# Performance work log

Hardware: AMD Instinct MI355X
Metric: run time of the kernel (lower is better)

The kernel has to match this reference:

```python
import jax, jax.numpy as jnp
import numpy as np

NH = 4        # n_head
L_TOPK = 16   # AWG top-k l
DEC = 2       # dec_layers
EPS = 1e-6


def _ln(x, g, b):
    m = jnp.mean(x, -1, keepdims=True)
    v = jnp.mean((x - m) ** 2, -1, keepdims=True)
    return (x - m) * jax.lax.rsqrt(v + EPS) * g + b


def _heads(x, W):
    B, L, C = x.shape
    return (x @ W).reshape(B, L, NH, C // NH).transpose(0, 2, 1, 3)  # [B,H,L,dk]


def _softmax_attn(qh, kh):
    dk = qh.shape[-1]
    logits = jnp.einsum('bhqd,bhkd->bhqk', qh / jnp.sqrt(jnp.float32(dk)), kh)
    return jax.nn.softmax(logits, axis=-1)


def cross_attn_block(q, k, v, Wq, Wk, Wv, Wo, g, b):
    B, Lq, C = q.shape
    a = _softmax_attn(_heads(q, Wq), _heads(k, Wk))
    o = jnp.einsum('bhqk,bhkd->bhqd', a, _heads(v, Wv))
    o = o.transpose(0, 2, 1, 3).reshape(B, Lq, C) @ Wo
    return _ln(o + q, g, b)


def awg_attn_block(q, k, v, Wq, Wk, Wv, Wo, g, b):
    # top-k attention-weight-gating: keep weights >= l-th largest, renormalize
    B, Lq, C = q.shape
    a = _softmax_attn(_heads(q, Wq), _heads(k, Wk))
    thr = jax.lax.top_k(a, L_TOPK)[0][..., -1:]          # [B,H,Lq,1]
    w = a * (a >= thr).astype(a.dtype)
    w = w / jnp.sum(w, -1, keepdims=True)
    o = jnp.einsum('bhqk,bhkd->bhqd', w, _heads(v, Wv))
    o = o.transpose(0, 2, 1, 3).reshape(B, Lq, C) @ Wo
    return _ln(o + q, g, b)


def setup_inputs() -> dict:
    key = jax.random.key(0)
    ks = jax.random.split(key, 32)
    B, Lq, Lk, C, F = 4, 3000, 750, 64, 256
    s = 1.0 / np.sqrt(C)
    sf = 1.0 / np.sqrt(F)
    d = {}
    d['q'] = jax.random.normal(ks[0], (B, Lq, C), jnp.float32)
    d['enc'] = jax.random.normal(ks[1], (B, Lk, C), jnp.float32)
    # cross_attn_layer params
    for i, n in enumerate(['cal_Wq', 'cal_Wk', 'cal_Wv', 'cal_Wo']):
        d[n] = jax.random.normal(ks[2 + i], (C, C), jnp.float32) * s
    d['cal_ln1_g'] = jnp.ones((C,), jnp.float32)
    d['cal_ln1_b'] = jnp.zeros((C,), jnp.float32)
    d['cal_W1'] = jax.random.normal(ks[6], (C, F), jnp.float32) * s
    d['cal_b1'] = jnp.zeros((F,), jnp.float32)
    d['cal_W2'] = jax.random.normal(ks[7], (F, C), jnp.float32) * sf
    d['cal_b2'] = jnp.zeros((C,), jnp.float32)
    d['cal_ln2_g'] = jnp.ones((C,), jnp.float32)
    d['cal_ln2_b'] = jnp.zeros((C,), jnp.float32)
    # stacked MGAN params [DEC, ...]
    d['m_ln_g'] = jnp.ones((DEC, C), jnp.float32)
    d['m_ln_b'] = jnp.zeros((DEC, C), jnp.float32)
    d['m_fc1_W'] = jax.random.normal(ks[8], (DEC, C, C), jnp.float32) * s
    d['m_fc1_b'] = jnp.zeros((DEC, C), jnp.float32)
    d['m_fc2_W'] = jax.random.normal(ks[9], (DEC, C, C), jnp.float32) * s
    d['m_fc2_b'] = jnp.zeros((DEC, C), jnp.float32)
    for i, n in enumerate(['m_Wq', 'm_Wk', 'm_Wv', 'm_Wo']):
        d[n] = jax.random.normal(ks[10 + i], (DEC, C, C), jnp.float32) * s
    d['m_aln_g'] = jnp.ones((DEC, C), jnp.float32)
    d['m_aln_b'] = jnp.zeros((DEC, C), jnp.float32)
    d['fc_W'] = jax.random.normal(ks[14], (C, 1), jnp.float32) * s
    d['fc_b'] = jnp.zeros((1,), jnp.float32)
    return d


def reference(q, enc, cal_Wq, cal_Wk, cal_Wv, cal_Wo, cal_ln1_g, cal_ln1_b,
              cal_W1, cal_b1, cal_W2, cal_b2, cal_ln2_g, cal_ln2_b,
              m_ln_g, m_ln_b, m_fc1_W, m_fc1_b, m_fc2_W, m_fc2_b,
              m_Wq, m_Wk, m_Wv, m_Wo, m_aln_g, m_aln_b, fc_W, fc_b):
    # cross_attn_layer: attention + FFN + LN (dropout = identity in eval)
    x = cross_attn_block(q, enc, enc, cal_Wq, cal_Wk, cal_Wv, cal_Wo, cal_ln1_g, cal_ln1_b)
    ffn = jax.nn.relu(x @ cal_W1 + cal_b1) @ cal_W2 + cal_b2
    x = _ln(ffn + x, cal_ln2_g, cal_ln2_b)
    # MGAN decoder layers (rep_KV: k,v = encoder output)
    for i in range(DEC):
        qn = _ln(x, m_ln_g[i], m_ln_b[i])
        sg = jax.nn.sigmoid(qn @ m_fc1_W[i] + m_fc1_b[i]) * (qn @ m_fc2_W[i] + m_fc2_b[i])
        awg = awg_attn_block(sg, enc, enc, m_Wq[i], m_Wk[i], m_Wv[i], m_Wo[i],
                             m_aln_g[i], m_aln_b[i])
        # GLU(cat(sg, awg)) = sg * sigmoid(awg)
        x = qn + sg * jax.nn.sigmoid(awg)
    # label_type='p' head
    return jax.nn.sigmoid(x @ fc_W + fc_b)  # [B, Lq, 1]
```

## Files before the change

### kernel.cpp

```cpp
#include <hip/hip_runtime.h>
#include <hip/hip_bf16.h>

using bf16 = __hip_bfloat16;

#define DEV_INLINE __device__ __forceinline__

constexpr int B_  = 4;
constexpr int LQ  = 3000;
constexpr int LK  = 750;
constexpr int NH_ = 4;
constexpr float EPSF = 1e-6f;

constexpr int PITCH = 753;

constexpr size_t WS_KV = 0;
constexpr size_t WS_XB = 1152000;
constexpr size_t WS_QP = 1920000;
constexpr size_t WS_AO = 2688000;
constexpr size_t WS_QN = 3456000;
constexpr size_t WS_SG = 4224000;

typedef _Float16 half2_t __attribute__((ext_vector_type(2)));
typedef _Float16 half4_t __attribute__((ext_vector_type(4)));
typedef float    f32x4   __attribute__((ext_vector_type(4)));

#define MFMA16(a, b, c) __builtin_amdgcn_mfma_f32_16x16x16f16((a), (b), (c), 0, 0, 0)

DEV_INLINE float sigmoidf(float x) { return 1.f / (1.f + __expf(-x)); }

DEV_INLINE unsigned int packh2(float a, float b) {
  half2_t h = { (_Float16)a, (_Float16)b };
  unsigned int u; __builtin_memcpy(&u, &h, 4); return u;
}
DEV_INLINE half2_t u2h(unsigned int u) {
  half2_t h; __builtin_memcpy(&h, &u, 4); return h;
}
DEV_INLINE unsigned short f2h(float f) {
  _Float16 h = (_Float16)f;
  unsigned short u; __builtin_memcpy(&u, &h, 2); return u;
}
DEV_INLINE half4_t h4_from(const unsigned short* p) {
  unsigned int lo = *(const unsigned int*)p;
  unsigned int hi = *(const unsigned int*)(p + 2);
  unsigned long long v = ((unsigned long long)hi << 32) | lo;
  half4_t h; __builtin_memcpy(&h, &v, 8); return h;
}
DEV_INLINE float dot2(unsigned int kw, half2_t qh, float acc) {
  return __builtin_amdgcn_fdot2(u2h(kw), qh, acc, false);
}

DEV_INLINE unsigned int f2sort(float f) {
  int ib = __float_as_int(f);
  return (unsigned int)(ib ^ ((ib >> 31) | 0x80000000));
}
DEV_INLINE float sort2f(unsigned int u) {
  const int ib = (u & 0x80000000u) ? (int)(u ^ 0x80000000u) : (int)~u;
  return __int_as_float(ib);
}

DEV_INLINE unsigned int bcastu(unsigned int v) {
  return (unsigned int)__builtin_amdgcn_readfirstlane((int)v);
}

DEV_INLINE void sort64u_desc4(unsigned int v[4]) {
  const int lane = threadIdx.x & 63;
  #pragma unroll
  for (int k = 2; k <= 64; k <<= 1) {
    #pragma unroll
    for (int j = k >> 1; j > 0; j >>= 1) {
      const bool takeMax = ((lane & j) == 0) == ((lane & k) == 0);
      #pragma unroll
      for (int r = 0; r < 4; ++r) {
        const unsigned int o = __shfl_xor(v[r], j);
        v[r] = (takeMax == (v[r] > o)) ? v[r] : o;
      }
    }
  }
}
DEV_INLINE void sort64p_desc4(unsigned long long v[4]) {
  const int lane = threadIdx.x & 63;
  #pragma unroll
  for (int k = 2; k <= 64; k <<= 1) {
    #pragma unroll
    for (int j = k >> 1; j > 0; j >>= 1) {
      const bool takeMax = ((lane & j) == 0) == ((lane & k) == 0);
      #pragma unroll
      for (int r = 0; r < 4; ++r) {
        const unsigned long long o = __shfl_xor(v[r], j);
        v[r] = (takeMax == (v[r] > o)) ? v[r] : o;
      }
    }
  }
}

DEV_INLINE float row_ln(float v, float g, float b) {
  float s1 = v, s2 = v * v;
  #pragma unroll
  for (int off = 32; off > 0; off >>= 1) {
    s1 += __shfl_xor(s1, off);
    s2 += __shfl_xor(s2, off);
  }
  const float m   = s1 * (1.f / 64.f);
  const float var = s2 * (1.f / 64.f) - m * m;
  return (v - m) * rsqrtf(var + EPSF) * g + b;
}

__global__ __launch_bounds__(256) void kvq_proj_kernel(
    const float* __restrict__ enc, const float* __restrict__ q,
    const float* __restrict__ calWq,
    const float* __restrict__ calWk, const float* __restrict__ calWv,
    const float* __restrict__ mWk, const float* __restrict__ mWv,
    float* __restrict__ kv, float* __restrict__ qp)
{
  const int y = blockIdx.y;
  if (y < 6 && blockIdx.x >= 188) return;
  __shared__ float Wl[64 * 65];
  __shared__ float xs[16][64];
  const int t = threadIdx.x, rr = t >> 6, cc = t & 63;
  const float* W;
  const float* src;
  float* dst;
  float scale = 1.f;
  int nrows = 3000;
  switch (y) {
    case 0: W = calWk; src = enc; dst = kv;               break;
    case 1: W = calWv; src = enc; dst = kv + 192000;      break;
    case 2: W = mWk;        src = enc; dst = kv + 384000; break;
    case 3: W = mWv;        src = enc; dst = kv + 576000; break;
    case 4: W = mWk + 4096; src = enc; dst = kv + 768000; break;
    case 5: W = mWv + 4096; src = enc; dst = kv + 960000; break;
    default: W = calWq; src = q; dst = qp; scale = 0.25f; nrows = 12000; break;
  }
  const bool packK = (y == 2) || (y == 4);
  for (int i = t; i < 4096; i += 256) Wl[(i >> 6) * 65 + (i & 63)] = W[i];
  const int base = blockIdx.x * 16;
  for (int i = t; i < 1024; i += 256) {
    const int grow = base + (i >> 6);
    xs[i >> 6][i & 63] = (grow < nrows) ? src[(size_t)grow * 64 + (i & 63)] : 0.f;
  }
  __syncthreads();
  #pragma unroll
  for (int p = 0; p < 4; ++p) {
    const int row = p * 4 + rr;
    const int grow = base + row;
    float acc = 0.f;
    #pragma unroll
    for (int c = 0; c < 64; ++c) acc = fmaf(xs[row][c], Wl[c * 65 + cc], acc);
    if (packK) {
      const float accN = __shfl_xor(acc, 1);
      if (!(cc & 1) && grow < nrows)
        ((unsigned int*)dst)[(size_t)grow * 32 + (cc >> 1)] = packh2(acc, accN);
    } else if (grow < nrows) {
      dst[(size_t)grow * 64 + cc] = acc * scale;
    }
  }
}

__global__ __launch_bounds__(256) void cross_attn_kernel(
    const float* __restrict__ qp, const float* __restrict__ kp,
    const float* __restrict__ vp, float* __restrict__ ao)
{
  extern __shared__ char smem[];
  unsigned short* Kl = (unsigned short*)smem;
  unsigned short* Vt = Kl + 750 * 18;
  unsigned short* Pt = Vt + 16 * 754;

  const int t = threadIdx.x;
  const int h = blockIdx.y, b = blockIdx.z;
  const float* kslab = kp + (size_t)(b * LK) * 64 + h * 16;
  const float* vslab = vp + (size_t)(b * LK) * 64 + h * 16;

  for (int k = t; k < LK; k += 256) {
    const float4* ks = (const float4*)(kslab + (size_t)k * 64);
    const float4* vs = (const float4*)(vslab + (size_t)k * 64);
    unsigned int* kr = (unsigned int*)(Kl + k * 18);
    #pragma unroll
    for (int q4 = 0; q4 < 4; ++q4) {
      float4 a = ks[q4], v = vs[q4];
      kr[q4 * 2]     = packh2(a.x, a.y);
      kr[q4 * 2 + 1] = packh2(a.z, a.w);
      Vt[(q4 * 4 + 0) * 754 + k] = f2h(v.x);
      Vt[(q4 * 4 + 1) * 754 + k] = f2h(v.y);
      Vt[(q4 * 4 + 2) * 754 + k] = f2h(v.z);
      Vt[(q4 * 4 + 3) * 754 + k] = f2h(v.w);
    }
  }
  if (t < 32) Vt[(t & 15) * 754 + 750 + (t >> 4)] = 0;
  __syncthreads();

  const int wave = t >> 6, lane = t & 63;
  const int col = lane & 15, quad = lane >> 4;
  const int qbase = blockIdx.x * 64 + wave * 16;
  unsigned short* Pt_w = Pt + wave * 288;

  int qrow = qbase + col; if (qrow >= LQ) qrow = LQ - 1;
  const float* qptr = qp + ((size_t)(b * LQ + qrow)) * 64 + h * 16 + quad * 4;
  half4_t aQ;
  {
    unsigned long long v = ((unsigned long long)packh2(qptr[2], qptr[3]) << 32)
                         | packh2(qptr[0], qptr[1]);
    __builtin_memcpy(&aQ, &v, 8);
  }

  f32x4 O = {0.f, 0.f, 0.f, 0.f};
  float Zp[4] = {0.f, 0.f, 0.f, 0.f};
  const f32x4 zeroC = {0.f, 0.f, 0.f, 0.f};

  for (int tile = 0; tile < 47; ++tile) {
    const int key = tile * 16 + col;
    const half4_t bK = h4_from(Kl + key * 18 + quad * 4);
    f32x4 S = MFMA16(aQ, bK, zeroC);
    const bool valid = key < LK;
    float e0 = valid ? __expf(S[0]) : 0.f;
    float e1 = valid ? __expf(S[1]) : 0.f;
    float e2 = valid ? __expf(S[2]) : 0.f;
    float e3 = valid ? __expf(S[3]) : 0.f;
    Zp[0] += e0; Zp[1] += e1; Zp[2] += e2; Zp[3] += e3;
    Pt_w[(quad * 4 + 0) * 18 + col] = f2h(e0);
    Pt_w[(quad * 4 + 1) * 18 + col] = f2h(e1);
    Pt_w[(quad * 4 + 2) * 18 + col] = f2h(e2);
    Pt_w[(quad * 4 + 3) * 18 + col] = f2h(e3);
    const half4_t aP = h4_from(Pt_w + col * 18 + quad * 4);
    const half4_t bV = h4_from(Vt + col * 754 + tile * 16 + quad * 4);
    O = MFMA16(aP, bV, O);
  }

  #pragma unroll
  for (int r = 0; r < 4; ++r) {
    float z = Zp[r];
    z += __shfl_xor(z, 1);
    z += __shfl_xor(z, 2);
    z += __shfl_xor(z, 4);
    z += __shfl_xor(z, 8);
    Zp[r] = z;
  }

  #pragma unroll
  for (int r = 0; r < 4; ++r) {
    const int orow = qbase + quad * 4 + r;
    if (orow < LQ)
      ao[((size_t)(b * LQ + orow)) * 64 + h * 16 + col] = O[r] / Zp[r];
  }
}

__global__ __launch_bounds__(512) void awg_attn_kernel(
    const float* __restrict__ qp, const unsigned int* __restrict__ kp,
    const float* __restrict__ vp, float* __restrict__ ao)
{
  extern __shared__ char smem[];
  uint2*              KT2  = (uint2*)smem;
  unsigned long long* cand = (unsigned long long*)(smem + 4 * PITCH * 8);
  float*              selW = (float*)(smem + 4 * PITCH * 8 + 16384);
  unsigned short*     selK = (unsigned short*)(smem + 4 * PITCH * 8 + 16384 + 3072);

  const int t = threadIdx.x;
  const int h = blockIdx.y, b = blockIdx.z;
  const unsigned int* kslab = kp + ((size_t)(b * LK)) * 32 + h * 8;

  for (int k = t; k < LK; k += 512) {
    const uint2* ks = (const uint2*)(kslab + (size_t)k * 32);
    #pragma unroll
    for (int d4 = 0; d4 < 4; ++d4) KT2[d4 * PITCH + k] = ks[d4];
  }
  __syncthreads();

  const int wave = t >> 6, lane = t & 63;
  const unsigned long long below = (1ull << lane) - 1ull;
  unsigned long long* cd = cand + wave * 256;
  float*              sW = selW + wave * 96;
  unsigned short*     sK = selK + wave * 96;

  sW[lane] = -3.0e38f; sK[lane] = 0;
  if (lane < 32) { sW[64 + lane] = -3.0e38f; sK[64 + lane] = 0; }
  #pragma unroll
  for (int r = 0; r < 4; ++r) cd[r * 64 + lane] = 0ull;

  const int r0 = blockIdx.x * 32 + wave * 4;
  int r0r = r0; if (r0r > LQ - 4) r0r = LQ - 4;
  const float* qrow = qp + ((size_t)(b * LQ + r0r)) * 64 + h * 16;
  unsigned int qw[4][8];
  #pragma unroll
  for (int r = 0; r < 4; ++r) {
    #pragma unroll
    for (int i = 0; i < 8; ++i)
      qw[r][i] = bcastu(packh2(qrow[r * 64 + 2 * i], qrow[r * 64 + 2 * i + 1]));
  }

  float lg[4][12];
  #pragma unroll
  for (int tt = 0; tt < 12; ++tt) {
    const int k = lane + (tt << 6);
    if (tt < 11 || k < LK) {
      float a0 = 0.f, a1 = 0.f, a2 = 0.f, a3 = 0.f;
      #pragma unroll
      for (int d4 = 0; d4 < 4; ++d4) {
        const uint2 w = KT2[d4 * PITCH + k];
        a0 = dot2(w.x, u2h(qw[0][2 * d4]), a0); a0 = dot2(w.y, u2h(qw[0][2 * d4 + 1]), a0);
        a1 = dot2(w.x, u2h(qw[1][2 * d4]), a1); a1 = dot2(w.y, u2h(qw[1][2 * d4 + 1]), a1);
        a2 = dot2(w.x, u2h(qw[2][2 * d4]), a2); a2 = dot2(w.y, u2h(qw[2][2 * d4 + 1]), a2);
        a3 = dot2(w.x, u2h(qw[3][2 * d4]), a3); a3 = dot2(w.y, u2h(qw[3][2 * d4 + 1]), a3);
      }
      lg[0][tt] = a0; lg[1][tt] = a1; lg[2][tt] = a2; lg[3][tt] = a3;
    } else {
      lg[0][tt] = -3.0e38f; lg[1][tt] = -3.0e38f;
      lg[2][tt] = -3.0e38f; lg[3][tt] = -3.0e38f;
    }
  }

  unsigned int hs[4];
  #pragma unroll
  for (int r = 0; r < 4; ++r) {
    float m = lg[r][0];
    #pragma unroll
    for (int tt = 1; tt < 12; ++tt) m = fmaxf(m, lg[r][tt]);
    hs[r] = f2sort(m);
  }

  sort64u_desc4(hs);
  unsigned int L[4];
  #pragma unroll
  for (int r = 0; r < 4; ++r) L[r] = __shfl(hs[r], 15);

  int cb[4] = {0, 0, 0, 0};
  #pragma unroll
  for (int tt = 0; tt < 12; ++tt) {
    const int k = lane + (tt << 6);
    #pragma unroll
    for (int r = 0; r < 4; ++r) {
      const unsigned int s = f2sort(lg[r][tt]);
      const bool p = s >= L[r];
      const unsigned long long m = __ballot(p);
      if (p) {
        const int pos = cb[r] + (int)__popcll(m & below);
        if (pos < 64)
          cd[r * 64 + pos] = ((unsigned long long)s << 16) | (unsigned int)k;
      }
      cb[r] += (int)__popcll(m);
    }
  }

  unsigned long long sv[4];
  #pragma unroll
  for (int r = 0; r < 4; ++r) sv[r] = cd[r * 64 + lane];
  sort64p_desc4(sv);

  unsigned int su[4], cu15[4];
  float Mv[4];
  #pragma unroll
  for (int r = 0; r < 4; ++r) {
    su[r]   = (unsigned int)(sv[r] >> 16);
    cu15[r] = __shfl(su[r], 15);
    Mv[r]   = sort2f(__shfl(su[r], 0));
  }
  #pragma unroll
  for (int r = 0; r < 4; ++r) {
    if (lane < 24 && su[r] >= cu15[r]) {
      sW[r * 24 + lane] = sort2f(su[r]);
      sK[r * 24 + lane] = (unsigned short)(sv[r] & 0xFFFFull);
    }
  }

  const int dd = lane & 15;
  const int rsel = lane >> 4;
  const float ref = (rsel == 0) ? Mv[0] : (rsel == 1) ? Mv[1] : (rsel == 2) ? Mv[2] : Mv[3];
  const float* cwr = sW + rsel * 24;
  const unsigned short* cir = sK + rsel * 24;
  const float* vbase = vp + (size_t)(b * LK) * 64 + h * 16 + dd;
  float acc = 0.f, Z = 0.f;
  #pragma unroll
  for (int j = 0; j < 24; ++j) {
    const float e = __expf(cwr[j] - ref);
    Z += e;
    acc = fmaf(e, vbase[(size_t)cir[j] * 64], acc);
  }
  if (r0 + rsel < LQ)
    ao[((size_t)(b * LQ + r0 + rsel)) * 64 + h * 16 + dd] = acc / Z;
}

__global__ __launch_bounds__(256) void cross_ffn_kernel(
    const float* __restrict__ ao, const float* __restrict__ qres,
    const float* __restrict__ Wo,
    const float* __restrict__ g1, const float* __restrict__ b1n,
    const float* __restrict__ W1, const float* __restrict__ bb1,
    const float* __restrict__ W2, const float* __restrict__ bb2,
    const float* __restrict__ g2, const float* __restrict__ b2n,
    float* __restrict__ xout)
{
  __shared__ float xs[8][64];
  __shared__ float hs[8][256];
  const int t = threadIdx.x, rr = t >> 6, cc = t & 63;
  const size_t base = (size_t)blockIdx.x * 8;
  for (int i = t; i < 512; i += 256) xs[i >> 6][i & 63] = ao[base * 64 + i];
  __syncthreads();
  float acc[2];
  #pragma unroll
  for (int p = 0; p < 2; ++p) {
    const int row = p * 4 + rr;
    float a = 0.f;
    #pragma unroll
    for (int c = 0; c < 64; ++c) a = fmaf(xs[row][c], Wo[c * 64 + cc], a);
    acc[p] = a + qres[(base + row) * 64 + cc];
  }
  __syncthreads();
  #pragma unroll
  for (int p = 0; p < 2; ++p) {
    const int row = p * 4 + rr;
    xs[row][cc] = row_ln(acc[p], g1[cc], b1n[cc]);
  }
  __syncthreads();
  {
    float hv[8];
    #pragma unroll
    for (int r = 0; r < 8; ++r) hv[r] = 0.f;
    #pragma unroll 8
    for (int c = 0; c < 64; ++c) {
      const float w = W1[c * 256 + t];
      #pragma unroll
      for (int r = 0; r < 8; ++r) hv[r] = fmaf(xs[r][c], w, hv[r]);
    }
    const float bb = bb1[t];
    #pragma unroll
    for (int r = 0; r < 8; ++r) hs[r][t] = fmaxf(hv[r] + bb, 0.f);
  }
  __syncthreads();
  float acc2[2];
  #pragma unroll
  for (int p = 0; p < 2; ++p) acc2[p] = bb2[cc];
  #pragma unroll 8
  for (int c = 0; c < 256; ++c) {
    const float w = W2[c * 64 + cc];
    acc2[0] = fmaf(hs[rr][c], w, acc2[0]);
    acc2[1] = fmaf(hs[4 + rr][c], w, acc2[1]);
  }
  #pragma unroll
  for (int p = 0; p < 2; ++p) {
    const int row = p * 4 + rr;
    const float a = acc2[p] + xs[row][cc];
    xout[(base + row) * 64 + cc] = row_ln(a, g2[cc], b2n[cc]);
  }
}

__global__ __launch_bounds__(256) void mgan_pre_kernel(
    const float* __restrict__ x, const float* __restrict__ lng,
    const float* __restrict__ lnb, const float* __restrict__ W1,
    const float* __restrict__ bb1, const float* __restrict__ W2,
    const float* __restrict__ bb2, const float* __restrict__ Wq,
    float* __restrict__ qn, float* __restrict__ sg, float* __restrict__ qp)
{
  __shared__ float qs[8][64];
  __shared__ float sgs[8][64];
  const int t = threadIdx.x, rr = t >> 6, cc = t & 63;
  const size_t base = (size_t)blockIdx.x * 8;
  #pragma unroll
  for (int p = 0; p < 2; ++p) {
    const int row = p * 4 + rr;
    const float v = x[(base + row) * 64 + cc];
    const float qv = row_ln(v, lng[cc], lnb[cc]);
    qn[(base + row) * 64 + cc] = qv;
    qs[row][cc] = qv;
  }
  __syncthreads();
  float d1[2], d2[2];
  #pragma unroll
  for (int p = 0; p < 2; ++p) { d1[p] = bb1[cc]; d2[p] = bb2[cc]; }
  #pragma unroll 4
  for (int c = 0; c < 64; ++c) {
    const float w1 = W1[c * 64 + cc];
    const float w2 = W2[c * 64 + cc];
    #pragma unroll
    for (int p = 0; p < 2; ++p) {
      const float xv = qs[p * 4 + rr][c];
      d1[p] = fmaf(xv, w1, d1[p]);
      d2[p] = fmaf(xv, w2, d2[p]);
    }
  }
  #pragma unroll
  for (int p = 0; p < 2; ++p) {
    const int row = p * 4 + rr;
    const float sv = sigmoidf(d1[p]) * d2[p];
    sg[(base + row) * 64 + cc] = sv;
    sgs[row][cc] = sv;
  }
  __syncthreads();
  #pragma unroll
  for (int p = 0; p < 2; ++p) {
    const int row = p * 4 + rr;
    float a = 0.f;
    #pragma unroll
    for (int c = 0; c < 64; ++c) a = fmaf(sgs[row][c], Wq[c * 64 + cc], a);
    qp[(base + row) * 64 + cc] = a * 0.25f;
  }
}

__global__ __launch_bounds__(256) void out_pre_kernel(
    const float* __restrict__ ao, const float* __restrict__ sg,
    const float* __restrict__ qn, const float* __restrict__ Wo,
    const float* __restrict__ g_, const float* __restrict__ b_,
    const float* __restrict__ lng, const float* __restrict__ lnb,
    const float* __restrict__ W1, const float* __restrict__ bb1,
    const float* __restrict__ W2, const float* __restrict__ bb2,
    const float* __restrict__ Wq,
    float* __restrict__ qn_out, float* __restrict__ sg_out,
    float* __restrict__ qp_out)
{
  __shared__ float xs[8][64];
  __shared__ float sgs[8][64];
  const int t = threadIdx.x, rr = t >> 6, cc = t & 63;
  const size_t base = (size_t)blockIdx.x * 8;
  for (int i = t; i < 512; i += 256) xs[i >> 6][i & 63] = ao[base * 64 + i];
  __syncthreads();
  float accp[2], sgv[2];
  #pragma unroll
  for (int p = 0; p < 2; ++p) {
    const int row = p * 4 + rr;
    const size_t idx = (base + row) * 64 + cc;
    float a = 0.f;
    #pragma unroll
    for (int c = 0; c < 64; ++c) a = fmaf(xs[row][c], Wo[c * 64 + cc], a);
    sgv[p] = sg[idx];
    accp[p] = a + sgv[p];
  }
  __syncthreads();
  #pragma unroll
  for (int p = 0; p < 2; ++p) {
    const int row = p * 4 + rr;
    const size_t idx = (base + row) * 64 + cc;
    const float awg = row_ln(accp[p], g_[cc], b_[cc]);
    const float xv = qn[idx] + sgv[p] * sigmoidf(awg);
    const float qv = row_ln(xv, lng[cc], lnb[cc]);
    qn_out[idx] = qv;
    xs[row][cc] = qv;
  }
  __syncthreads();
  float d1[2], d2[2];
  #pragma unroll
  for (int p = 0; p < 2; ++p) { d1[p] = bb1[cc]; d2[p] = bb2[cc]; }
  #pragma unroll 4
  for (int c = 0; c < 64; ++c) {
    const float w1 = W1[c * 64 + cc];
    const float w2 = W2[c * 64 + cc];
    #pragma unroll
    for (int p = 0; p < 2; ++p) {
      const float xv = xs[p * 4 + rr][c];
      d1[p] = fmaf(xv, w1, d1[p]);
      d2[p] = fmaf(xv, w2, d2[p]);
    }
  }
  __syncthreads();
  #pragma unroll
  for (int p = 0; p < 2; ++p) {
    const int row = p * 4 + rr;
    const size_t idx = (base + row) * 64 + cc;
    const float sv = sigmoidf(d1[p]) * d2[p];
    sg_out[idx] = sv;
    sgs[row][cc] = sv;
  }
  __syncthreads();
  #pragma unroll
  for (int p = 0; p < 2; ++p) {
    const int row = p * 4 + rr;
    float a = 0.f;
    #pragma unroll
    for (int c = 0; c < 64; ++c) a = fmaf(sgs[row][c], Wq[c * 64 + cc], a);
    qp_out[(base + row) * 64 + cc] = a * 0.25f;
  }
}

__global__ __launch_bounds__(256) void out_final_kernel(
    const float* __restrict__ ao, const float* __restrict__ sg,
    const float* __restrict__ qn, const float* __restrict__ Wo,
    const float* __restrict__ g_, const float* __restrict__ b_,
    const float* __restrict__ fw, const float* __restrict__ fb,
    float* __restrict__ out)
{
  __shared__ float xs[8][64];
  const int t = threadIdx.x, rr = t >> 6, cc = t & 63;
  const size_t base = (size_t)blockIdx.x * 8;
  for (int i = t; i < 512; i += 256) xs[i >> 6][i & 63] = ao[base * 64 + i];
  __syncthreads();
  #pragma unroll
  for (int p = 0; p < 2; ++p) {
    const int row = p * 4 + rr;
    const size_t idx = (base + row) * 64 + cc;
    float a = 0.f;
    #pragma unroll
    for (int c = 0; c < 64; ++c) a = fmaf(xs[row][c], Wo[c * 64 + cc], a);
    const float sgv = sg[idx];
    a += sgv;
    const float awg = row_ln(a, g_[cc], b_[cc]);
    const float xv = qn[idx] + sgv * sigmoidf(awg);
    float v = xv * fw[cc];
    #pragma unroll
    for (int off = 32; off > 0; off >>= 1) v += __shfl_xor(v, off);
    if (cc == 0) out[base + row] = sigmoidf(v + fb[0]);
  }
}

extern "C" void kernel_launch(void* const* d_in, const int* in_sizes, int n_in,
                              void* d_out, int out_size, void* d_ws, size_t ws_size,
                              hipStream_t stream) {
  (void)in_sizes; (void)n_in; (void)out_size; (void)ws_size;

  const float* q     = (const float*)d_in[0];
  const float* enc   = (const float*)d_in[1];
  const float* calWq = (const float*)d_in[2];
  const float* calWk = (const float*)d_in[3];
  const float* calWv = (const float*)d_in[4];
  const float* calWo = (const float*)d_in[5];
  const float* ln1g  = (const float*)d_in[6];
  const float* ln1b  = (const float*)d_in[7];
  const float* W1    = (const float*)d_in[8];
  const float* b1v   = (const float*)d_in[9];
  const float* W2    = (const float*)d_in[10];
  const float* b2v   = (const float*)d_in[11];
  const float* ln2g  = (const float*)d_in[12];
  const float* ln2b  = (const float*)d_in[13];
  const float* mlng  = (const float*)d_in[14];
  const float* mlnb  = (const float*)d_in[15];
  const float* mfc1W = (const float*)d_in[16];
  const float* mfc1b = (const float*)d_in[17];
  const float* mfc2W = (const float*)d_in[18];
  const float* mfc2b = (const float*)d_in[19];
  const float* mWq   = (const float*)d_in[20];
  const float* mWk   = (const float*)d_in[21];
  const float* mWv   = (const float*)d_in[22];
  const float* mWo   = (const float*)d_in[23];
  const float* malng = (const float*)d_in[24];
  const float* malnb = (const float*)d_in[25];
  const float* fcW   = (const float*)d_in[26];
  const float* fcb   = (const float*)d_in[27];
  float* out = (float*)d_out;

  float* ws  = (float*)d_ws;
  float* kv  = ws + WS_KV;
  float* qp  = ws + WS_QP;
  float* aob = ws + WS_AO;
  float* qnb = ws + WS_QN;
  float* sgb = ws + WS_SG;
  float* xb  = ws + WS_XB;

  const size_t crossLds = (750 * 18 + 16 * 754 + 4 * 288) * 2;
  const size_t awgLds   = 4 * PITCH * 8 + 16384 + 3072 + 1536;

  kvq_proj_kernel<<<dim3(750, 7), 256, 0, stream>>>(enc, q, calWq, calWk, calWv,
                                                    mWk, mWv, kv, qp);

  cross_attn_kernel<<<dim3(47, NH_, B_), 256, crossLds, stream>>>(qp, kv, kv + 192000, aob);
  cross_ffn_kernel<<<1500, 256, 0, stream>>>(aob, q, calWo, ln1g, ln1b,
                                             W1, b1v, W2, b2v, ln2g, ln2b, xb);

  mgan_pre_kernel<<<1500, 256, 0, stream>>>(xb, mlng, mlnb, mfc1W, mfc1b,
                                            mfc2W, mfc2b, mWq, qnb, sgb, qp);
  awg_attn_kernel<<<dim3(94, NH_, B_), 512, awgLds, stream>>>(
      qp, (const unsigned int*)(kv + 2 * 192000), kv + 3 * 192000, aob);
  out_pre_kernel<<<1500, 256, 0, stream>>>(aob, sgb, qnb, mWo, malng, malnb,
                                           mlng + 64, mlnb + 64,
                                           mfc1W + 4096, mfc1b + 64,
                                           mfc2W + 4096, mfc2b + 64,
                                           mWq + 4096, qnb, sgb, qp);

  awg_attn_kernel<<<dim3(94, NH_, B_), 512, awgLds, stream>>>(
      qp, (const unsigned int*)(kv + 4 * 192000), kv + 5 * 192000, aob);
  out_final_kernel<<<1500, 256, 0, stream>>>(aob, sgb, qnb, mWo + 4096,
                                             malng + 64, malnb + 64, fcW, fcb, out);
}
```

Baseline: 360.0 us.

## Fuse cross FFN with MGAN pre, split candidate arrays, shrink row blocks

Merges the cross-attention FFN kernel with the first MGAN pre-processing kernel, which removes one launch and the round trip of the intermediate x buffer through global memory. The row-wise kernels now handle 4 rows per block instead of 8, doubling the block count. In the AWG top-k selection, 64-bit packed candidates are split into separate 32-bit value and 16-bit index arrays, so the bitonic sort runs on 32-bit keys and ballot compaction picks the winners. The LDS pitch also changes from 753 to 751. Sorting on values alone can change which keys are kept when candidates tie, and the smaller blocks reuse each loaded weight across fewer rows.

Result: slower. 393.9 us (+9.4%).

```diff
diff --git a/kernel.cpp b/kernel.cpp
--- a/kernel.cpp
+++ b/kernel.cpp
@@ -11,7 +11,7 @@
 constexpr int NH_ = 4;
 constexpr float EPSF = 1e-6f;
 
-constexpr int PITCH = 753;
+constexpr int PITCH = 751;
 
 constexpr size_t WS_KV = 0;
 constexpr size_t WS_XB = 1152000;
@@ -72,21 +72,6 @@
       #pragma unroll
       for (int r = 0; r < 4; ++r) {
         const unsigned int o = __shfl_xor(v[r], j);
-        v[r] = (takeMax == (v[r] > o)) ? v[r] : o;
-      }
-    }
-  }
-}
-DEV_INLINE void sort64p_desc4(unsigned long long v[4]) {
-  const int lane = threadIdx.x & 63;
-  #pragma unroll
-  for (int k = 2; k <= 64; k <<= 1) {
-    #pragma unroll
-    for (int j = k >> 1; j > 0; j >>= 1) {
-      const bool takeMax = ((lane & j) == 0) == ((lane & k) == 0);
-      #pragma unroll
-      for (int r = 0; r < 4; ++r) {
-        const unsigned long long o = __shfl_xor(v[r], j);
         v[r] = (takeMax == (v[r] > o)) ? v[r] : o;
       }
     }
@@ -248,10 +233,11 @@
     const float* __restrict__ vp, float* __restrict__ ao)
 {
   extern __shared__ char smem[];
-  uint2*              KT2  = (uint2*)smem;
-  unsigned long long* cand = (unsigned long long*)(smem + 4 * PITCH * 8);
-  float*              selW = (float*)(smem + 4 * PITCH * 8 + 16384);
-  unsigned short*     selK = (unsigned short*)(smem + 4 * PITCH * 8 + 16384 + 3072);
+  uint2*          KT2   = (uint2*)smem;
+  unsigned int*   candV = (unsigned int*)(smem + 4 * PITCH * 8);
+  unsigned short* candK = (unsigned short*)(smem + 4 * PITCH * 8 + 8192);
+  float*          selW  = (float*)(smem + 4 * PITCH * 8 + 8192 + 4096);
+  unsigned short* selK  = (unsigned short*)(smem + 4 * PITCH * 8 + 8192 + 4096 + 3072);
 
   const int t = threadIdx.x;
   const int h = blockIdx.y, b = blockIdx.z;
@@ -266,14 +252,15 @@
 
   const int wave = t >> 6, lane = t & 63;
   const unsigned long long below = (1ull << lane) - 1ull;
-  unsigned long long* cd = cand + wave * 256;
-  float*              sW = selW + wave * 96;
-  unsigned short*     sK = selK + wave * 96;
+  unsigned int*   cV = candV + wave * 256;
+  unsigned short* cK = candK + wave * 256;
+  float*          sW = selW + wave * 96;
+  unsigned short* sK = selK + wave * 96;
 
   sW[lane] = -3.0e38f; sK[lane] = 0;
   if (lane < 32) { sW[64 + lane] = -3.0e38f; sK[64 + lane] = 0; }
   #pragma unroll
-  for (int r = 0; r < 4; ++r) cd[r * 64 + lane] = 0ull;
+  for (int r = 0; r < 4; ++r) cV[r * 64 + lane] = 0u;
 
   const int r0 = blockIdx.x * 32 + wave * 4;
   int r0r = r0; if (r0r > LQ - 4) r0r = LQ - 4;
@@ -332,31 +319,30 @@
       const unsigned long long m = __ballot(p);
       if (p) {
         const int pos = cb[r] + (int)__popcll(m & below);
-        if (pos < 64)
-          cd[r * 64 + pos] = ((unsigned long long)s << 16) | (unsigned int)k;
+        if (pos < 64) { cV[r * 64 + pos] = s; cK[r * 64 + pos] = (unsigned short)k; }
       }
       cb[r] += (int)__popcll(m);
     }
   }
 
-  unsigned long long sv[4];
-  #pragma unroll
-  for (int r = 0; r < 4; ++r) sv[r] = cd[r * 64 + lane];
-  sort64p_desc4(sv);
-
-  unsigned int su[4], cu15[4];
-  float Mv[4];
+  unsigned int su[4], so[4];
+  #pragma unroll
+  for (int r = 0; r < 4; ++r) { su[r] = cV[r * 64 + lane]; so[r] = su[r]; }
+  sort64u_desc4(so);
+  unsigned int T[4]; float Mv[4];
   #pragma unroll
   for (int r = 0; r < 4; ++r) {
-    su[r]   = (unsigned int)(sv[r] >> 16);
-    cu15[r] = __shfl(su[r], 15);
-    Mv[r]   = sort2f(__shfl(su[r], 0));
-  }
+    T[r]  = __shfl(so[r], 15);
+    Mv[r] = sort2f(__shfl(so[r], 0));
+  }
+
   #pragma unroll
   for (int r = 0; r < 4; ++r) {
-    if (lane < 24 && su[r] >= cu15[r]) {
-      sW[r * 24 + lane] = sort2f(su[r]);
-      sK[r * 24 + lane] = (unsigned short)(sv[r] & 0xFFFFull);
+    const bool w = su[r] >= T[r];
+    const unsigned long long mw = __ballot(w);
+    if (w) {
+      const int pos = (int)__popcll(mw & below);
+      if (pos < 24) { sW[r * 24 + pos] = sort2f(su[r]); sK[r * 24 + pos] = cK[r * 64 + lane]; }
     }
   }
 
@@ -377,119 +363,72 @@
     ao[((size_t)(b * LQ + r0 + rsel)) * 64 + h * 16 + dd] = acc / Z;
 }
 
-__global__ __launch_bounds__(256) void cross_ffn_kernel(
+__global__ __launch_bounds__(256) void ffn_pre_kernel(
     const float* __restrict__ ao, const float* __restrict__ qres,
     const float* __restrict__ Wo,
     const float* __restrict__ g1, const float* __restrict__ b1n,
     const float* __restrict__ W1, const float* __restrict__ bb1,
     const float* __restrict__ W2, const float* __restrict__ bb2,
     const float* __restrict__ g2, const float* __restrict__ b2n,
-    float* __restrict__ xout)
+    const float* __restrict__ lng, const float* __restrict__ lnb,
+    const float* __restrict__ fc1W, const float* __restrict__ fc1b,
+    const float* __restrict__ fc2W, const float* __restrict__ fc2b,
+    const float* __restrict__ Wq,
+    float* __restrict__ qn, float* __restrict__ sg, float* __restrict__ qp)
 {
-  __shared__ float xs[8][64];
-  __shared__ float hs[8][256];
+  __shared__ float xs[4][64];
+  __shared__ float hsm[4][256];
   const int t = threadIdx.x, rr = t >> 6, cc = t & 63;
-  const size_t base = (size_t)blockIdx.x * 8;
-  for (int i = t; i < 512; i += 256) xs[i >> 6][i & 63] = ao[base * 64 + i];
-  __syncthreads();
-  float acc[2];
-  #pragma unroll
-  for (int p = 0; p < 2; ++p) {
-    const int row = p * 4 + rr;
-    float a = 0.f;
-    #pragma unroll
-    for (int c = 0; c < 64; ++c) a = fmaf(xs[row][c], Wo[c * 64 + cc], a);
-    acc[p] = a + qres[(base + row) * 64 + cc];
-  }
-  __syncthreads();
-  #pragma unroll
-  for (int p = 0; p < 2; ++p) {
-    const int row = p * 4 + rr;
-    xs[row][cc] = row_ln(acc[p], g1[cc], b1n[cc]);
-  }
+  const size_t base = (size_t)blockIdx.x * 4;
+  const size_t idx = (base + rr) * 64 + cc;
+  xs[rr][cc] = ao[idx];
+  __syncthreads();
+  float a = 0.f;
+  #pragma unroll
+  for (int c = 0; c < 64; ++c) a = fmaf(xs[rr][c], Wo[c * 64 + cc], a);
+  a += qres[idx];
+  __syncthreads();
+  const float x1 = row_ln(a, g1[cc], b1n[cc]);
+  xs[rr][cc] = x1;
   __syncthreads();
   {
-    float hv[8];
-    #pragma unroll
-    for (int r = 0; r < 8; ++r) hv[r] = 0.f;
+    float hv[4] = {0.f, 0.f, 0.f, 0.f};
     #pragma unroll 8
     for (int c = 0; c < 64; ++c) {
       const float w = W1[c * 256 + t];
       #pragma unroll
-      for (int r = 0; r < 8; ++r) hv[r] = fmaf(xs[r][c], w, hv[r]);
+      for (int r = 0; r < 4; ++r) hv[r] = fmaf(xs[r][c], w, hv[r]);
     }
     const float bb = bb1[t];
     #pragma unroll
-    for (int r = 0; r < 8; ++r) hs[r][t] = fmaxf(hv[r] + bb, 0.f);
-  }
-  __syncthreads();
-  float acc2[2];
-  #pragma unroll
-  for (int p = 0; p < 2; ++p) acc2[p] = bb2[cc];
+    for (int r = 0; r < 4; ++r) hsm[r][t] = fmaxf(hv[r] + bb, 0.f);
+  }
+  __syncthreads();
+  float a2 = bb2[cc];
   #pragma unroll 8
-  for (int c = 0; c < 256; ++c) {
-    const float w = W2[c * 64 + cc];
-    acc2[0] = fmaf(hs[rr][c], w, acc2[0]);
-    acc2[1] = fmaf(hs[4 + rr][c], w, acc2[1]);
-  }
-  #pragma unroll
-  for (int p = 0; p < 2; ++p) {
-    const int row = p * 4 + rr;
-    const float a = acc2[p] + xs[row][cc];
-    xout[(base + row) * 64 + cc] = row_ln(a, g2[cc], b2n[cc]);
-  }
-}
-
-__global__ __launch_bounds__(256) void mgan_pre_kernel(
-    const float* __restrict__ x, const float* __restrict__ lng,
-    const float* __restrict__ lnb, const float* __restrict__ W1,
-    const float* __restrict__ bb1, const float* __restrict__ W2,
-    const float* __restrict__ bb2, const float* __restrict__ Wq,
-    float* __restrict__ qn, float* __restrict__ sg, float* __restrict__ qp)
-{
-  __shared__ float qs[8][64];
-  __shared__ float sgs[8][64];
-  const int t = threadIdx.x, rr = t >> 6, cc = t & 63;
-  const size_t base = (size_t)blockIdx.x * 8;
-  #pragma unroll
-  for (int p = 0; p < 2; ++p) {
-    const int row = p * 4 + rr;
-    const float v = x[(base + row) * 64 + cc];
-    const float qv = row_ln(v, lng[cc], lnb[cc]);
-    qn[(base + row) * 64 + cc] = qv;
-    qs[row][cc] = qv;
-  }
-  __syncthreads();
-  float d1[2], d2[2];
-  #pragma unroll
-  for (int p = 0; p < 2; ++p) { d1[p] = bb1[cc]; d2[p] = bb2[cc]; }
+  for (int c = 0; c < 256; ++c) a2 = fmaf(hsm[rr][c], W2[c * 64 + cc], a2);
+  const float xv = row_ln(a2 + x1, g2[cc], b2n[cc]);
+  const float qv = row_ln(xv, lng[cc], lnb[cc]);
+  qn[idx] = qv;
+  __syncthreads();
+  xs[rr][cc] = qv;
+  __syncthreads();
+  float d1 = fc1b[cc], d2 = fc2b[cc];
   #pragma unroll 4
   for (int c = 0; c < 64; ++c) {
-    const float w1 = W1[c * 64 + cc];
-    const float w2 = W2[c * 64 + cc];
-    #pragma unroll
-    for (int p = 0; p < 2; ++p) {
-      const float xv = qs[p * 4 + rr][c];
-      d1[p] = fmaf(xv, w1, d1[p]);
-      d2[p] = fmaf(xv, w2, d2[p]);
-    }
-  }
-  #pragma unroll
-  for (int p = 0; p < 2; ++p) {
-    const int row = p * 4 + rr;
-    const float sv = sigmoidf(d1[p]) * d2[p];
-    sg[(base + row) * 64 + cc] = sv;
-    sgs[row][cc] = sv;
-  }
-  __syncthreads();
-  #pragma unroll
-  for (int p = 0; p < 2; ++p) {
-    const int row = p * 4 + rr;
-    float a = 0.f;
-    #pragma unroll
-    for (int c = 0; c < 64; ++c) a = fmaf(sgs[row][c], Wq[c * 64 + cc], a);
-    qp[(base + row) * 64 + cc] = a * 0.25f;
-  }
+    const float xq = xs[rr][c];
+    d1 = fmaf(xq, fc1W[c * 64 + cc], d1);
+    d2 = fmaf(xq, fc2W[c * 64 + cc], d2);
+  }
+  const float sv = sigmoidf(d1) * d2;
+  sg[idx] = sv;
+  __syncthreads();
+  xs[rr][cc] = sv;
+  __syncthreads();
+  float aq = 0.f;
+  #pragma unroll
+  for (int c = 0; c < 64; ++c) aq = fmaf(xs[rr][c], Wq[c * 64 + cc], aq);
+  qp[idx] = aq * 0.25f;
 }
 
 __global__ __launch_bounds__(256) void out_pre_kernel(
@@ -503,67 +442,40 @@
     float* __restrict__ qn_out, float* __restrict__ sg_out,
     float* __restrict__ qp_out)
 {
-  __shared__ float xs[8][64];
-  __shared__ float sgs[8][64];
+  __shared__ float xs[4][64];
   const int t = threadIdx.x, rr = t >> 6, cc = t & 63;
-  const size_t base = (size_t)blockIdx.x * 8;
-  for (int i = t; i < 512; i += 256) xs[i >> 6][i & 63] = ao[base * 64 + i];
-  __syncthreads();
-  float accp[2], sgv[2];
-  #pragma unroll
-  for (int p = 0; p < 2; ++p) {
-    const int row = p * 4 + rr;
-    const size_t idx = (base + row) * 64 + cc;
-    float a = 0.f;
-    #pragma unroll
-    for (int c = 0; c < 64; ++c) a = fmaf(xs[row][c], Wo[c * 64 + cc], a);
-    sgv[p] = sg[idx];
-    accp[p] = a + sgv[p];
-  }
-  __syncthreads();
-  #pragma unroll
-  for (int p = 0; p < 2; ++p) {
-    const int row = p * 4 + rr;
-    const size_t idx = (base + row) * 64 + cc;
-    const float awg = row_ln(accp[p], g_[cc], b_[cc]);
-    const float xv = qn[idx] + sgv[p] * sigmoidf(awg);
-    const float qv = row_ln(xv, lng[cc], lnb[cc]);
-    qn_out[idx] = qv;
-    xs[row][cc] = qv;
-  }
-  __syncthreads();
-  float d1[2], d2[2];
-  #pragma unroll
-  for (int p = 0; p < 2; ++p) { d1[p] = bb1[cc]; d2[p] = bb2[cc]; }
+  const size_t base = (size_t)blockIdx.x * 4;
+  const size_t idx = (base + rr) * 64 + cc;
+  xs[rr][cc] = ao[idx];
+  __syncthreads();
+  float a = 0.f;
+  #pragma unroll
+  for (int c = 0; c < 64; ++c) a = fmaf(xs[rr][c], Wo[c * 64 + cc], a);
+  const float sgv = sg[idx];
+  a += sgv;
+  __syncthreads();
+  const float awg = row_ln(a, g_[cc], b_[cc]);
+  const float xv = qn[idx] + sgv * sigmoidf(awg);
+  const float qv = row_ln(xv, lng[cc], lnb[cc]);
+  qn_out[idx] = qv;
+  xs[rr][cc] = qv;
+  __syncthreads();
+  float d1 = bb1[cc], d2 = bb2[cc];
   #pragma unroll 4
   for (int c = 0; c < 64; ++c) {
-    const float w1 = W1[c * 64 + cc];
-    const float w2 = W2[c * 64 + cc];
-    #pragma unroll
-    for (int p = 0; p < 2; ++p) {
-      const float xv = xs[p * 4 + rr][c];
-      d1[p] = fmaf(xv, w1, d1[p]);
-      d2[p] = fmaf(xv, w2, d2[p]);
-    }
-  }
-  __syncthreads();
-  #pragma unroll
-  for (int p = 0; p < 2; ++p) {
-    const int row = p * 4 + rr;
-    const size_t idx = (base + row) * 64 + cc;
-    const float sv = sigmoidf(d1[p]) * d2[p];
-    sg_out[idx] = sv;
-    sgs[row][cc] = sv;
-  }
-  __syncthreads();
-  #pragma unroll
-  for (int p = 0; p < 2; ++p) {
-    const int row = p * 4 + rr;
-    float a = 0.f;
-    #pragma unroll
-    for (int c = 0; c < 64; ++c) a = fmaf(sgs[row][c], Wq[c * 64 + cc], a);
-    qp_out[(base + row) * 64 + cc] = a * 0.25f;
-  }
+    const float xq = xs[rr][c];
+    d1 = fmaf(xq, W1[c * 64 + cc], d1);
+    d2 = fmaf(xq, W2[c * 64 + cc], d2);
+  }
+  const float sv = sigmoidf(d1) * d2;
+  sg_out[idx] = sv;
+  __syncthreads();
+  xs[rr][cc] = sv;
+  __syncthreads();
+  float aq = 0.f;
+  #pragma unroll
+  for (int c = 0; c < 64; ++c) aq = fmaf(xs[rr][c], Wq[c * 64 + cc], aq);
+  qp_out[idx] = aq * 0.25f;
 }
 
 __global__ __launch_bounds__(256) void out_final_kernel(
@@ -573,27 +485,23 @@
     const float* __restrict__ fw, const float* __restrict__ fb,
     float* __restrict__ out)
 {
-  __shared__ float xs[8][64];
+  __shared__ float xs[4][64];
   const int t = threadIdx.x, rr = t >> 6, cc = t & 63;
-  const size_t base = (size_t)blockIdx.x * 8;
-  for (int i = t; i < 512; i += 256) xs[i >> 6][i & 63] = ao[base * 64 + i];
-  __syncthreads();
-  #pragma unroll
-  for (int p = 0; p < 2; ++p) {
-    const int row = p * 4 + rr;
-    const size_t idx = (base + row) * 64 + cc;
-    float a = 0.f;
-    #pragma unroll
-    for (int c = 0; c < 64; ++c) a = fmaf(xs[row][c], Wo[c * 64 + cc], a);
-    const float sgv = sg[idx];
-    a += sgv;
-    const float awg = row_ln(a, g_[cc], b_[cc]);
-    const float xv = qn[idx] + sgv * sigmoidf(awg);
-    float v = xv * fw[cc];
-    #pragma unroll
-    for (int off = 32; off > 0; off >>= 1) v += __shfl_xor(v, off);
-    if (cc == 0) out[base + row] = sigmoidf(v + fb[0]);
-  }
+  const size_t base = (size_t)blockIdx.x * 4;
+  const size_t idx = (base + rr) * 64 + cc;
+  xs[rr][cc] = ao[idx];
+  __syncthreads();
+  float a = 0.f;
+  #pragma unroll
+  for (int c = 0; c < 64; ++c) a = fmaf(xs[rr][c], Wo[c * 64 + cc], a);
+  const float sgv = sg[idx];
+  a += sgv;
+  const float awg = row_ln(a, g_[cc], b_[cc]);
+  const float xv = qn[idx] + sgv * sigmoidf(awg);
+  float v = xv * fw[cc];
+  #pragma unroll
+  for (int off = 32; off > 0; off >>= 1) v += __shfl_xor(v, off);
+  if (cc == 0) out[base + rr] = sigmoidf(v + fb[0]);
 }
 
 extern "C" void kernel_launch(void* const* d_in, const int* in_sizes, int n_in,
@@ -637,23 +545,22 @@
   float* aob = ws + WS_AO;
   float* qnb = ws + WS_QN;
   float* sgb = ws + WS_SG;
-  float* xb  = ws + WS_XB;
 
   const size_t crossLds = (750 * 18 + 16 * 754 + 4 * 288) * 2;
-  const size_t awgLds   = 4 * PITCH * 8 + 16384 + 3072 + 1536;
+  const size_t awgLds   = 4 * PITCH * 8 + 8192 + 4096 + 3072 + 1536;
 
   kvq_proj_kernel<<<dim3(750, 7), 256, 0, stream>>>(enc, q, calWq, calWk, calWv,
                                                     mWk, mWv, kv, qp);
 
   cross_attn_kernel<<<dim3(47, NH_, B_), 256, crossLds, stream>>>(qp, kv, kv + 192000, aob);
-  cross_ffn_kernel<<<1500, 256, 0, stream>>>(aob, q, calWo, ln1g, ln1b,
-                                             W1, b1v, W2, b2v, ln2g, ln2b, xb);
-
-  mgan_pre_kernel<<<1500, 256, 0, stream>>>(xb, mlng, mlnb, mfc1W, mfc1b,
-                                            mfc2W, mfc2b, mWq, qnb, sgb, qp);
+  ffn_pre_kernel<<<3000, 256, 0, stream>>>(aob, q, calWo, ln1g, ln1b,
+                                           W1, b1v, W2, b2v, ln2g, ln2b,
+                                           mlng, mlnb, mfc1W, mfc1b,
+                                           mfc2W, mfc2b, mWq, qnb, sgb, qp);
+
   awg_attn_kernel<<<dim3(94, NH_, B_), 512, awgLds, stream>>>(
       qp, (const unsigned int*)(kv + 2 * 192000), kv + 3 * 192000, aob);
-  out_pre_kernel<<<1500, 256, 0, stream>>>(aob, sgb, qnb, mWo, malng, malnb,
+  out_pre_kernel<<<3000, 256, 0, stream>>>(aob, sgb, qnb, mWo, malng, malnb,
                                            mlng + 64, mlnb + 64,
                                            mfc1W + 4096, mfc1b + 64,
                                            mfc2W + 4096, mfc2b + 64,
@@ -661,6 +568,6 @@
 
   awg_attn_kernel<<<dim3(94, NH_, B_), 512, awgLds, stream>>>(
       qp, (const unsigned int*)(kv + 4 * 192000), kv + 5 * 192000, aob);
-  out_final_kernel<<<1500, 256, 0, stream>>>(aob, sgb, qnb, mWo + 4096,
+  out_final_kernel<<<3000, 256, 0, stream>>>(aob, sgb, qnb, mWo + 4096,
                                              malng + 64, malnb + 64, fcW, fcb, out);
 }
```
